# Kernel tuning notes

Measured on AMD Instinct MI355X. Metric: run time of the kernel, lower is better.

Reference implementation:

```python
import jax, jax.numpy as jnp
import numpy as np

K = 16  # top-k patches kept (module default)

def setup_inputs() -> dict:
    key = jax.random.key(0)
    ks = jax.random.split(key, 5)
    N, D, A, H = 100000, 1024, 128, 256
    x = jax.random.normal(ks[0], (N, D), dtype=jnp.float32)
    Wa1 = jax.random.normal(ks[1], (D, A), dtype=jnp.float32) * (1.0 / np.sqrt(D))
    ba1 = jnp.zeros((A,), dtype=jnp.float32)
    Wa2 = jax.random.normal(ks[2], (A, 1), dtype=jnp.float32) * (1.0 / np.sqrt(A))
    ba2 = jnp.zeros((1,), dtype=jnp.float32)
    Wc1 = jax.random.normal(ks[3], (D, H), dtype=jnp.float32) * (1.0 / np.sqrt(D))
    bc1 = jnp.zeros((H,), dtype=jnp.float32)
    Wc2 = jax.random.normal(ks[4], (H, 1), dtype=jnp.float32) * (1.0 / np.sqrt(H))
    bc2 = jnp.zeros((1,), dtype=jnp.float32)
    return {"x": x, "Wa1": Wa1, "ba1": ba1, "Wa2": Wa2, "ba2": ba2,
            "Wc1": Wc1, "bc1": bc1, "Wc2": Wc2, "bc2": bc2}

def reference(x, Wa1, ba1, Wa2, ba2, Wc1, bc1, Wc2, bc2):
    # attention logits: Linear -> tanh -> Linear, shape [N]
    scores = (jnp.tanh(x @ Wa1 + ba1) @ Wa2 + ba2)[:, 0]
    # top-k selection over patch dim (k < N here)
    top_vals, top_idx = jax.lax.top_k(scores, K)       # [K], [K]
    x_k = x[top_idx]                                    # [K, D] gather
    attn_w = jax.nn.softmax(top_vals)                   # renormalise over k
    slide_embedding = attn_w @ x_k                      # [D] weighted sum
    # classifier MLP (dropout is identity in eval)
    h = jax.nn.relu(slide_embedding @ Wc1 + bc1)
    logit = (h @ Wc2 + bc2)[0]
    # scatter attention weights back into full-length vector
    full_weights = jnp.zeros(x.shape[0], dtype=x.dtype).at[top_idx].set(attn_w)
    return logit, slide_embedding, full_weights, top_idx
```

## Files before the change

### kernel.cpp

```cpp
#include <hip/hip_runtime.h>
#include <cstddef>
#include <cstdint>

#define N_PATCH 100000
#define D_IN    1024
#define A_DIM   128
#define H_DIM   256
#define KTOP    16

#define OUT_LOGIT 0
#define OUT_EMB   1
#define OUT_FW    (1 + D_IN)
#define OUT_TOPI  (OUT_FW + N_PATCH)

#define WS_SCORES 0
#define WS_CANDV  (N_PATCH)
#define WS_CANDI  (N_PATCH + 4096)
#define WS_ATTN   (N_PATCH + 2 * 4096)
#define WS_TOPI   (WS_ATTN + KTOP)
#define WS_EMB    (WS_TOPI + KTOP)
#define WS_HPART  (WS_EMB + D_IN)
#define WS_WPK    (WS_HPART + 16 * H_DIM)

#define NB2A  256
#define CHUNK 391

typedef __attribute__((ext_vector_type(8))) short bf8_t;
typedef __attribute__((ext_vector_type(4))) float f4_t;

__global__ __launch_bounds__(256) void k_prepack(
    const float* __restrict__ Wa1, uint4* __restrict__ wpk)
{
    int t = blockIdx.x * 256 + threadIdx.x;
    int lane = t & 63;
    int part = (t >> 6) & 1;
    int nt   = (t >> 7) & 7;
    int ks   = t >> 10;
    int n  = nt * 16 + (lane & 15);
    int k0 = ks * 32 + ((lane >> 4) * 8);
    union { ushort u[8]; uint4 v; } o;
    #pragma unroll
    for (int j = 0; j < 8; ++j) {
        float w = Wa1[(size_t)(k0 + j) * A_DIM + n];
        uint b = __float_as_uint(w);
        if (part == 0) {
            o.u[j] = (ushort)(b >> 16);
        } else {
            float hf = __uint_as_float(b & 0xffff0000u);
            o.u[j] = (ushort)(__float_as_uint(w - hf) >> 16);
        }
    }
    wpk[t] = o.v;
}

__device__ __forceinline__ void split8(const float4& a, const float4& b,
                                       bf8_t& hi, bf8_t& lo)
{
    float f[8] = {a.x, a.y, a.z, a.w, b.x, b.y, b.z, b.w};
    union { ushort u[8]; bf8_t v; } H, L;
    #pragma unroll
    for (int j = 0; j < 8; ++j) {
        uint t = __float_as_uint(f[j]);
        H.u[j] = (ushort)(t >> 16);
        float hf = __uint_as_float(t & 0xffff0000u);
        L.u[j] = (ushort)(__float_as_uint(f[j] - hf) >> 16);
    }
    hi = H.v; lo = L.v;
}

__global__ __launch_bounds__(256) void k_scores(
    const float* __restrict__ x, const uint4* __restrict__ wpk,
    const float* __restrict__ ba1, const float* __restrict__ Wa2,
    const float* __restrict__ ba2, float* __restrict__ scores)
{
    __shared__ uint4 sB[1024];

    const int tid = threadIdx.x;
    const int ln  = tid & 63;
    const int q   = ln >> 4;
    const int c   = ln & 15;
    const int wv  = tid >> 6;
    const int row0 = blockIdx.x * 128 + wv * 32;

    const int r0 = min(row0 + c,      N_PATCH - 1);
    const int r1 = min(row0 + 16 + c, N_PATCH - 1);
    const float* pa0 = x + (size_t)r0 * D_IN + q * 8;
    const float* pa1 = x + (size_t)r1 * D_IN + q * 8;

    f4_t acc[2][8];
    #pragma unroll
    for (int rt = 0; rt < 2; ++rt)
        #pragma unroll
        for (int nt = 0; nt < 8; ++nt)
            acc[rt][nt] = (f4_t){0.f, 0.f, 0.f, 0.f};

    uint4 bpre[4];
    #pragma unroll
    for (int i = 0; i < 4; ++i) bpre[i] = wpk[tid + i * 256];

    for (int ks = 0; ks < 32; ++ks) {
        __syncthreads();
        #pragma unroll
        for (int i = 0; i < 4; ++i) sB[tid + i * 256] = bpre[i];

        const float4 a0l = *(const float4*)(pa0 + ks * 32);
        const float4 a0h = *(const float4*)(pa0 + ks * 32 + 4);
        const float4 a1l = *(const float4*)(pa1 + ks * 32);
        const float4 a1h = *(const float4*)(pa1 + ks * 32 + 4);

        __syncthreads();

        if (ks < 31) {
            #pragma unroll
            for (int i = 0; i < 4; ++i) bpre[i] = wpk[(ks + 1) * 1024 + tid + i * 256];
        }

        bf8_t ahi[2], alo[2];
        split8(a0l, a0h, ahi[0], alo[0]);
        split8(a1l, a1h, ahi[1], alo[1]);

        const bf8_t* sBf = (const bf8_t*)sB;
        #pragma unroll
        for (int nt = 0; nt < 8; ++nt) {
            bf8_t bh = sBf[(nt * 2 + 0) * 64 + ln];
            bf8_t bl = sBf[(nt * 2 + 1) * 64 + ln];
            acc[0][nt] = __builtin_amdgcn_mfma_f32_16x16x32_bf16(ahi[0], bh, acc[0][nt], 0, 0, 0);
            acc[0][nt] = __builtin_amdgcn_mfma_f32_16x16x32_bf16(alo[0], bh, acc[0][nt], 0, 0, 0);
            acc[0][nt] = __builtin_amdgcn_mfma_f32_16x16x32_bf16(ahi[0], bl, acc[0][nt], 0, 0, 0);
            acc[1][nt] = __builtin_amdgcn_mfma_f32_16x16x32_bf16(ahi[1], bh, acc[1][nt], 0, 0, 0);
            acc[1][nt] = __builtin_amdgcn_mfma_f32_16x16x32_bf16(alo[1], bh, acc[1][nt], 0, 0, 0);
            acc[1][nt] = __builtin_amdgcn_mfma_f32_16x16x32_bf16(ahi[1], bl, acc[1][nt], 0, 0, 0);
        }
    }

    float b1v[8], w2v[8];
    #pragma unroll
    for (int nt = 0; nt < 8; ++nt) {
        b1v[nt] = ba1[nt * 16 + c];
        w2v[nt] = Wa2[nt * 16 + c];
    }
    const float b2 = ba2[0];

    #pragma unroll
    for (int rt = 0; rt < 2; ++rt)
        #pragma unroll
        for (int reg = 0; reg < 4; ++reg) {
            float p = 0.f;
            #pragma unroll
            for (int nt = 0; nt < 8; ++nt)
                p += tanhf(acc[rt][nt][reg] + b1v[nt]) * w2v[nt];
            #pragma unroll
            for (int off = 1; off < 16; off <<= 1)
                p += __shfl_xor(p, off, 64);
            if (c == 0) {
                int row = row0 + rt * 16 + q * 4 + reg;
                if (row < N_PATCH) scores[row] = p + b2;
            }
        }
}

__global__ __launch_bounds__(256) void k_topk_local(
    const float* __restrict__ scores, float* __restrict__ candv,
    int* __restrict__ candi, float* __restrict__ out_fw)
{
    __shared__ float sv[512];
    __shared__ float rv[256];
    __shared__ int   rs[256];
    const int tid  = threadIdx.x;
    const int base = blockIdx.x * CHUNK;

    for (int i = tid; i < 512; i += 256) {
        int g = base + i;
        sv[i] = (i < CHUNK && g < N_PATCH) ? scores[g] : -1e30f;
    }
    for (int i = tid; i < CHUNK; i += 256) {
        int g = base + i;
        if (g < N_PATCH) out_fw[g] = 0.f;
    }
    __syncthreads();

    for (int r = 0; r < KTOP; ++r) {
        float v1 = sv[tid], v2 = sv[tid + 256];
        float bv; int bs;
        if (v2 > v1) { bv = v2; bs = tid + 256; } else { bv = v1; bs = tid; }
        rv[tid] = bv; rs[tid] = bs;
        __syncthreads();
        for (int off = 128; off > 0; off >>= 1) {
            if (tid < off) {
                float ov = rv[tid + off]; int os = rs[tid + off];
                if (ov > rv[tid] || (ov == rv[tid] && os < rs[tid])) {
                    rv[tid] = ov; rs[tid] = os;
                }
            }
            __syncthreads();
        }
        if (tid == 0) {
            int s = rs[0];
            candv[blockIdx.x * KTOP + r] = rv[0];
            candi[blockIdx.x * KTOP + r] = base + s;
            sv[s] = -1e30f;
        }
        __syncthreads();
    }
}

__global__ __launch_bounds__(256) void k_topk_global(
    const float* __restrict__ candv, const int* __restrict__ candi,
    float* __restrict__ out, float* __restrict__ ws_attn, int* __restrict__ ws_topi)
{
    __shared__ float cv[4096];
    __shared__ int   ci[4096];
    __shared__ float rv[256];
    __shared__ int   rgx[256];
    __shared__ int   rsl[256];
    __shared__ float topv[KTOP];
    __shared__ int   topi[KTOP];
    __shared__ float attn[KTOP];
    const int tid = threadIdx.x;

    for (int i = tid; i < 4096; i += 256) { cv[i] = candv[i]; ci[i] = candi[i]; }
    __syncthreads();

    for (int r = 0; r < KTOP; ++r) {
        float bv = -1e38f; int bg = 0x7fffffff; int bs = tid * 16;
        #pragma unroll
        for (int i = 0; i < 16; ++i) {
            int s = tid * 16 + i;
            float v = cv[s]; int g = ci[s];
            if (v > bv || (v == bv && g < bg)) { bv = v; bg = g; bs = s; }
        }
        rv[tid] = bv; rgx[tid] = bg; rsl[tid] = bs;
        __syncthreads();
        for (int off = 128; off > 0; off >>= 1) {
            if (tid < off) {
                if (rv[tid + off] > rv[tid] ||
                    (rv[tid + off] == rv[tid] && rgx[tid + off] < rgx[tid])) {
                    rv[tid] = rv[tid + off]; rgx[tid] = rgx[tid + off]; rsl[tid] = rsl[tid + off];
                }
            }
            __syncthreads();
        }
        if (tid == 0) {
            topv[r] = rv[0]; topi[r] = rgx[0]; cv[rsl[0]] = -1e30f;
        }
        __syncthreads();
    }

    if (tid == 0) {
        float mx = topv[0];
        float s = 0.f;
        for (int k2 = 0; k2 < KTOP; ++k2) {
            float e = expf(topv[k2] - mx);
            attn[k2] = e; s += e;
        }
        float inv = 1.f / s;
        for (int k2 = 0; k2 < KTOP; ++k2) attn[k2] *= inv;
    }
    __syncthreads();

    if (tid < KTOP) {
        out[OUT_TOPI + tid] = (float)topi[tid];
        out[OUT_FW + topi[tid]] = attn[tid];
        ws_attn[tid] = attn[tid];
        ws_topi[tid] = topi[tid];
    }
}

__global__ __launch_bounds__(256) void k_embed(
    const float* __restrict__ x, const float* __restrict__ attn,
    const int* __restrict__ topi, float* __restrict__ out, float* __restrict__ emb)
{
    __shared__ float a[KTOP];
    __shared__ int   ti[KTOP];
    if (threadIdx.x < KTOP) { a[threadIdx.x] = attn[threadIdx.x]; ti[threadIdx.x] = topi[threadIdx.x]; }
    __syncthreads();
    int d = blockIdx.x * 256 + threadIdx.x;
    float e = 0.f;
    #pragma unroll
    for (int k2 = 0; k2 < KTOP; ++k2)
        e = fmaf(a[k2], x[(size_t)ti[k2] * D_IN + d], e);
    out[OUT_EMB + d] = e;
    emb[d] = e;
}

__global__ __launch_bounds__(256) void k_mlp1(
    const float* __restrict__ emb, const float* __restrict__ Wc1,
    float* __restrict__ hpart)
{
    __shared__ float se[64];
    const int b = blockIdx.x, tid = threadIdx.x;
    if (tid < 64) se[tid] = emb[b * 64 + tid];
    __syncthreads();
    float p = 0.f;
    #pragma unroll 8
    for (int d = 0; d < 64; ++d)
        p = fmaf(se[d], Wc1[(size_t)(b * 64 + d) * H_DIM + tid], p);
    hpart[b * H_DIM + tid] = p;
}

__global__ __launch_bounds__(256) void k_logit(
    const float* __restrict__ hpart, const float* __restrict__ bc1,
    const float* __restrict__ Wc2, const float* __restrict__ bc2,
    float* __restrict__ out)
{
    __shared__ float red[256];
    const int tid = threadIdx.x;
    float h = bc1[tid];
    #pragma unroll
    for (int i = 0; i < 16; ++i) h += hpart[i * H_DIM + tid];
    h = fmaxf(h, 0.f) * Wc2[tid];
    red[tid] = h;
    __syncthreads();
    for (int off = 128; off > 0; off >>= 1) {
        if (tid < off) red[tid] += red[tid + off];
        __syncthreads();
    }
    if (tid == 0) out[OUT_LOGIT] = red[0] + bc2[0];
}

extern "C" void kernel_launch(void* const* d_in, const int* in_sizes, int n_in,
                              void* d_out, int out_size, void* d_ws, size_t ws_size,
                              hipStream_t stream)
{
    const float* x   = (const float*)d_in[0];
    const float* Wa1 = (const float*)d_in[1];
    const float* ba1 = (const float*)d_in[2];
    const float* Wa2 = (const float*)d_in[3];
    const float* ba2 = (const float*)d_in[4];
    const float* Wc1 = (const float*)d_in[5];
    const float* bc1 = (const float*)d_in[6];
    const float* Wc2 = (const float*)d_in[7];
    const float* bc2 = (const float*)d_in[8];
    float* out = (float*)d_out;
    float* ws  = (float*)d_ws;

    float* scores = ws + WS_SCORES;
    float* candv  = ws + WS_CANDV;
    int*   candi  = (int*)(ws + WS_CANDI);
    float* attn   = ws + WS_ATTN;
    int*   topi   = (int*)(ws + WS_TOPI);
    float* emb    = ws + WS_EMB;
    float* hpart  = ws + WS_HPART;
    uint4* wpk    = (uint4*)(ws + WS_WPK);

    dim3 blk(256);
    k_prepack<<<128, blk, 0, stream>>>(Wa1, wpk);
    k_scores<<<(N_PATCH + 127) / 128, blk, 0, stream>>>(x, wpk, ba1, Wa2, ba2, scores);
    k_topk_local<<<NB2A, blk, 0, stream>>>(scores, candv, candi, out + OUT_FW);
    k_topk_global<<<1, blk, 0, stream>>>(candv, candi, out, attn, topi);
    k_embed<<<4, blk, 0, stream>>>(x, attn, topi, out, emb);
    k_mlp1<<<16, blk, 0, stream>>>(emb, Wc1, hpart);
    k_logit<<<1, blk, 0, stream>>>(hpart, bc1, Wc2, bc2, out);
}
```

Before: 779.5 us.

## Double-buffer weight LDS and prefetch x tiles in score GEMM loop

The score kernel now keeps two LDS buffers for the packed Wa1 tiles, so it needs one barrier per k-step instead of two. The next step's x fragments are loaded into registers one iteration ahead, and the global weight prefetch runs two steps ahead. The bf16 hi/lo split uses byte-permute instructions to pack pairs, and the MFMA calls are reordered so that independent accumulators interleave and dependency stalls are hidden. In exchange the kernel uses twice the LDS and more registers, which may lower occupancy.

```diff
diff --git a/kernel.cpp b/kernel.cpp
--- a/kernel.cpp
+++ b/kernel.cpp
@@ -56,24 +56,28 @@
 __device__ __forceinline__ void split8(const float4& a, const float4& b,
                                        bf8_t& hi, bf8_t& lo)
 {
-    float f[8] = {a.x, a.y, a.z, a.w, b.x, b.y, b.z, b.w};
-    union { ushort u[8]; bf8_t v; } H, L;
-    #pragma unroll
-    for (int j = 0; j < 8; ++j) {
-        uint t = __float_as_uint(f[j]);
-        H.u[j] = (ushort)(t >> 16);
-        float hf = __uint_as_float(t & 0xffff0000u);
-        L.u[j] = (ushort)(__float_as_uint(f[j] - hf) >> 16);
+    union { float f[8]; uint u[8]; float4 v4[2]; } X;
+    X.v4[0] = a; X.v4[1] = b;
+    union { uint u[4]; bf8_t v; } H, L;
+    #pragma unroll
+    for (int j = 0; j < 4; ++j) {
+        uint x0 = X.u[2 * j], x1 = X.u[2 * j + 1];
+        H.u[j] = __builtin_amdgcn_perm(x1, x0, 0x07060302);
+        float l0 = X.f[2 * j]     - __uint_as_float(x0 & 0xffff0000u);
+        float l1 = X.f[2 * j + 1] - __uint_as_float(x1 & 0xffff0000u);
+        L.u[j] = __builtin_amdgcn_perm(__float_as_uint(l1), __float_as_uint(l0), 0x07060302);
     }
     hi = H.v; lo = L.v;
 }
+
+#define MFMA_BF16 __builtin_amdgcn_mfma_f32_16x16x32_bf16
 
 __global__ __launch_bounds__(256) void k_scores(
     const float* __restrict__ x, const uint4* __restrict__ wpk,
     const float* __restrict__ ba1, const float* __restrict__ Wa2,
     const float* __restrict__ ba2, float* __restrict__ scores)
 {
-    __shared__ uint4 sB[1024];
+    __shared__ uint4 sB[2][1024];
 
     const int tid = threadIdx.x;
     const int ln  = tid & 63;
@@ -94,43 +98,66 @@
         for (int nt = 0; nt < 8; ++nt)
             acc[rt][nt] = (f4_t){0.f, 0.f, 0.f, 0.f};
 
-    uint4 bpre[4];
-    #pragma unroll
-    for (int i = 0; i < 4; ++i) bpre[i] = wpk[tid + i * 256];
+    uint4 b0[4], bpre[4];
+    #pragma unroll
+    for (int i = 0; i < 4; ++i) b0[i] = wpk[tid + i * 256];
+    #pragma unroll
+    for (int i = 0; i < 4; ++i) sB[0][tid + i * 256] = b0[i];
+    #pragma unroll
+    for (int i = 0; i < 4; ++i) bpre[i] = wpk[1024 + tid + i * 256];
+
+    float4 a_cur[4], a_nxt[4];
+    a_cur[0] = *(const float4*)(pa0);
+    a_cur[1] = *(const float4*)(pa0 + 4);
+    a_cur[2] = *(const float4*)(pa1);
+    a_cur[3] = *(const float4*)(pa1 + 4);
+
+    __syncthreads();
 
     for (int ks = 0; ks < 32; ++ks) {
-        __syncthreads();
-        #pragma unroll
-        for (int i = 0; i < 4; ++i) sB[tid + i * 256] = bpre[i];
-
-        const float4 a0l = *(const float4*)(pa0 + ks * 32);
-        const float4 a0h = *(const float4*)(pa0 + ks * 32 + 4);
-        const float4 a1l = *(const float4*)(pa1 + ks * 32);
-        const float4 a1h = *(const float4*)(pa1 + ks * 32 + 4);
-
-        __syncthreads();
+        const int cur = ks & 1;
 
         if (ks < 31) {
             #pragma unroll
-            for (int i = 0; i < 4; ++i) bpre[i] = wpk[(ks + 1) * 1024 + tid + i * 256];
-        }
-
-        bf8_t ahi[2], alo[2];
-        split8(a0l, a0h, ahi[0], alo[0]);
-        split8(a1l, a1h, ahi[1], alo[1]);
-
-        const bf8_t* sBf = (const bf8_t*)sB;
-        #pragma unroll
-        for (int nt = 0; nt < 8; ++nt) {
-            bf8_t bh = sBf[(nt * 2 + 0) * 64 + ln];
-            bf8_t bl = sBf[(nt * 2 + 1) * 64 + ln];
-            acc[0][nt] = __builtin_amdgcn_mfma_f32_16x16x32_bf16(ahi[0], bh, acc[0][nt], 0, 0, 0);
-            acc[0][nt] = __builtin_amdgcn_mfma_f32_16x16x32_bf16(alo[0], bh, acc[0][nt], 0, 0, 0);
-            acc[0][nt] = __builtin_amdgcn_mfma_f32_16x16x32_bf16(ahi[0], bl, acc[0][nt], 0, 0, 0);
-            acc[1][nt] = __builtin_amdgcn_mfma_f32_16x16x32_bf16(ahi[1], bh, acc[1][nt], 0, 0, 0);
-            acc[1][nt] = __builtin_amdgcn_mfma_f32_16x16x32_bf16(alo[1], bh, acc[1][nt], 0, 0, 0);
-            acc[1][nt] = __builtin_amdgcn_mfma_f32_16x16x32_bf16(ahi[1], bl, acc[1][nt], 0, 0, 0);
-        }
+            for (int i = 0; i < 4; ++i) sB[cur ^ 1][tid + i * 256] = bpre[i];
+            a_nxt[0] = *(const float4*)(pa0 + (ks + 1) * 32);
+            a_nxt[1] = *(const float4*)(pa0 + (ks + 1) * 32 + 4);
+            a_nxt[2] = *(const float4*)(pa1 + (ks + 1) * 32);
+            a_nxt[3] = *(const float4*)(pa1 + (ks + 1) * 32 + 4);
+        }
+        if (ks < 30) {
+            #pragma unroll
+            for (int i = 0; i < 4; ++i) bpre[i] = wpk[(ks + 2) * 1024 + tid + i * 256];
+        }
+
+        bf8_t ahi0, alo0, ahi1, alo1;
+        split8(a_cur[0], a_cur[1], ahi0, alo0);
+        split8(a_cur[2], a_cur[3], ahi1, alo1);
+
+        const bf8_t* sBf = (const bf8_t*)sB[cur];
+        #pragma unroll
+        for (int nt = 0; nt < 8; nt += 2) {
+            bf8_t bh0 = sBf[(nt * 2 + 0) * 64 + ln];
+            bf8_t bl0 = sBf[(nt * 2 + 1) * 64 + ln];
+            bf8_t bh1 = sBf[(nt * 2 + 2) * 64 + ln];
+            bf8_t bl1 = sBf[(nt * 2 + 3) * 64 + ln];
+            acc[0][nt]     = MFMA_BF16(ahi0, bh0, acc[0][nt],     0, 0, 0);
+            acc[1][nt]     = MFMA_BF16(ahi1, bh0, acc[1][nt],     0, 0, 0);
+            acc[0][nt + 1] = MFMA_BF16(ahi0, bh1, acc[0][nt + 1], 0, 0, 0);
+            acc[1][nt + 1] = MFMA_BF16(ahi1, bh1, acc[1][nt + 1], 0, 0, 0);
+            acc[0][nt]     = MFMA_BF16(alo0, bh0, acc[0][nt],     0, 0, 0);
+            acc[1][nt]     = MFMA_BF16(alo1, bh0, acc[1][nt],     0, 0, 0);
+            acc[0][nt + 1] = MFMA_BF16(alo0, bh1, acc[0][nt + 1], 0, 0, 0);
+            acc[1][nt + 1] = MFMA_BF16(alo1, bh1, acc[1][nt + 1], 0, 0, 0);
+            acc[0][nt]     = MFMA_BF16(ahi0, bl0, acc[0][nt],     0, 0, 0);
+            acc[1][nt]     = MFMA_BF16(ahi1, bl0, acc[1][nt],     0, 0, 0);
+            acc[0][nt + 1] = MFMA_BF16(ahi0, bl1, acc[0][nt + 1], 0, 0, 0);
+            acc[1][nt + 1] = MFMA_BF16(ahi1, bl1, acc[1][nt + 1], 0, 0, 0);
+        }
+
+        #pragma unroll
+        for (int i = 0; i < 4; ++i) a_cur[i] = a_nxt[i];
+        __syncthreads();
     }
 
     float b1v[8], w2v[8];
```

Result: no change. 777.1 us (-0.3%).
